# Performance work log

Hardware: AMD Instinct MI355X
Metric: run time of the kernel (lower is better)

Reference implementation:

```python
import jax, jax.numpy as jnp
import numpy as np

PENETRATION_W = 10.0
STABILITY_W = 1.0
ENERGY_W = 0.1
MIN_DIST = 0.05

B, T, N, D = 16, 100, 128, 3

def setup_inputs() -> dict:
    key = jax.random.key(0)
    k1, k2, k3 = jax.random.split(key, 3)
    trajectories = jax.random.normal(k1, (B, T, N, D), dtype=jnp.float32)
    velocities = jax.random.normal(k2, (B, T, N, D), dtype=jnp.float32)
    forces = jax.random.normal(k3, (B, T, N, D), dtype=jnp.float32)
    return {"trajectories": trajectories, "velocities": velocities, "forces": forces}

def _penetration_loss(trajectories):
    b, t, n, _ = trajectories.shape
    pos = trajectories[..., :3]                                   # [B,T,N,3]
    diff = pos[:, :, :, None, :] - pos[:, :, None, :, :]          # [B,T,N,N,3]
    d2 = jnp.sum(diff * diff, axis=-1)                            # [B,T,N,N]
    mask = jnp.triu(jnp.ones((n, n), dtype=bool), k=1)            # strictly i<j
    # avoid sqrt(0) on diagonal for safe gradients; masked out below
    dist = jnp.sqrt(jnp.where(mask, d2, 1.0))
    pen = jax.nn.relu(MIN_DIST - dist) * mask                     # [B,T,N,N]
    # original: sum over (t, i<j) of mean over batch
    total = jnp.mean(jnp.sum(pen, axis=(1, 2, 3)))
    return total / (t * n * (n - 1) / 2)

def _stability_loss(velocities):
    return jnp.mean(jnp.linalg.norm(velocities[:, -5:], axis=-1))

def _energy_loss(positions, velocities, forces):
    kinetic_start = 0.5 * jnp.mean(jnp.sum(velocities[:, 0] ** 2, axis=-1))
    kinetic_end = 0.5 * jnp.mean(jnp.sum(velocities[:, -1] ** 2, axis=-1))
    displacements = positions[:, 1:] - positions[:, :-1]
    work = jnp.mean(jnp.sum(forces[:, :-1] * displacements, axis=-1))
    return jnp.abs(kinetic_end - kinetic_start - work)

def reference(trajectories, velocities, forces):
    loss = PENETRATION_W * _penetration_loss(trajectories)
    loss = loss + STABILITY_W * _stability_loss(velocities)
    loss = loss + ENERGY_W * _energy_loss(trajectories, velocities, forces)
    return loss
```

## Files before the change

### kernel.cpp

```cpp
#include <hip/hip_runtime.h>
#include <math.h>

constexpr int B = 16, T = 100, N = 128;
constexpr float MIN_DIST  = 0.05f;
constexpr float MIN_DIST2 = MIN_DIST * MIN_DIST;

constexpr int THREADS      = 256;
constexpr int PEN_BLOCKS   = B * T;
constexpr int MISC_BLOCKS  = 160;
constexpr int TOTAL_BLOCKS = PEN_BLOCKS + MISC_BLOCKS;

constexpr int PER_B = T * N * 3;
constexpr int PER_T = N * 3;

constexpr int WORK_V4_PER_B = (T - 1) * N * 3 / 4;
constexpr int WORK_V4 = B * WORK_V4_PER_B;
constexpr int KE_V4_PER_SLICE = N * 3 / 4;
constexpr int KE_V4  = 2 * B * KE_V4_PER_SLICE;
constexpr int STAB_V = B * 5 * N;
constexpr int MISC_TOTAL = WORK_V4 + STAB_V + KE_V4;

constexpr int WORK_N = B * (T - 1) * N;

constexpr int WORK_OFF = 1600, STAB_OFF = 1760, KE0_OFF = 1920, KE1_OFF = 2080;

__device__ __forceinline__ float wave_sum(float v) {
#pragma unroll
    for (int off = 32; off > 0; off >>= 1) v += __shfl_down(v, off, 64);
    return v;
}

__global__ __launch_bounds__(THREADS) void physics_fused(
    const float* __restrict__ traj, const float* __restrict__ vel,
    const float* __restrict__ frc, float* __restrict__ ws)
{
    __shared__ float4 spos[N];
    __shared__ float  sraw[PER_T];
    __shared__ float  red[4][4];

    const int tid  = threadIdx.x;
    const int bid  = blockIdx.x;
    const int lane = tid & 63;
    const int wv   = tid >> 6;

    if (bid >= MISC_BLOCKS) {
        const int pb = bid - MISC_BLOCKS;
        if (tid < PER_T / 4)
            ((float4*)sraw)[tid] = ((const float4*)traj)[pb * (PER_T / 4) + tid];
        __syncthreads();
        if (tid < N)
            spos[tid] = make_float4(sraw[tid * 3], sraw[tid * 3 + 1], sraw[tid * 3 + 2], 0.f);
        __syncthreads();

        const int i    = tid & (N - 1);
        const int half = tid >> 7;
        const float4 pi = spos[i];
        float s = 0.f;
        const int k0 = 1 + half * 32;
        const int k1 = 32 + half * 31;
#pragma unroll 8
        for (int k = k0; k <= k1; ++k) {
            const int j = (i + k) & (N - 1);
            const float4 pj = spos[j];
            const float dx = pi.x - pj.x, dy = pi.y - pj.y, dz = pi.z - pj.z;
            const float d2 = dx * dx + dy * dy + dz * dz;
            const bool h = d2 < MIN_DIST2;
            if (__builtin_expect(__any(h), 0))
                if (h) s += MIN_DIST - sqrtf(d2);
        }
        if (half) {
            const float4 pj = spos[(i + 64) & (N - 1)];
            const float dx = pi.x - pj.x, dy = pi.y - pj.y, dz = pi.z - pj.z;
            const float d2 = dx * dx + dy * dy + dz * dz;
            const bool h = (d2 < MIN_DIST2) & (i < 64);
            if (__builtin_expect(__any(h), 0))
                if (h) s += MIN_DIST - sqrtf(d2);
        }
        float w = wave_sum(s);
        if (lane == 0) red[0][wv] = w;
        __syncthreads();
        if (tid == 0)
            ws[pb] = red[0][0] + red[0][1] + red[0][2] + red[0][3];
    } else {
        const int mb = bid;
        const float4* t4 = (const float4*)traj;
        const float4* f4 = (const float4*)frc;
        const float4* v4 = (const float4*)vel;
        float sw = 0.f, ss = 0.f, k0 = 0.f, k1 = 0.f;
        const int stride = MISC_BLOCKS * THREADS;
        for (int v = mb * THREADS + tid; v < MISC_TOTAL; v += stride) {
            if (v < WORK_V4) {
                const int b = v / WORK_V4_PER_B;
                const int r = v - b * WORK_V4_PER_B;
                const int base = b * (PER_B / 4) + r;
                const float4 f  = f4[base];
                const float4 t0 = t4[base];
                const float4 t1 = t4[base + PER_T / 4];
                sw += f.x * (t1.x - t0.x) + f.y * (t1.y - t0.y)
                    + f.z * (t1.z - t0.z) + f.w * (t1.w - t0.w);
            } else if (v < WORK_V4 + STAB_V) {
                const int s2 = v - WORK_V4;
                const int b  = s2 / 640;
                const int r  = s2 - b * 640;
                const int e  = b * PER_B + 95 * PER_T + r * 3;
                const float vx = vel[e], vy = vel[e + 1], vz = vel[e + 2];
                ss += sqrtf(vx * vx + vy * vy + vz * vz);
            } else {
                const int s2    = v - WORK_V4 - STAB_V;
                const int which = s2 / 1536;
                const int rr    = s2 - which * 1536;
                const int b     = rr / KE_V4_PER_SLICE;
                const int r     = rr - b * KE_V4_PER_SLICE;
                const float4 q  = v4[b * (PER_B / 4) + which * (99 * PER_T / 4) + r];
                const float k   = q.x * q.x + q.y * q.y + q.z * q.z + q.w * q.w;
                if (which) k1 += k; else k0 += k;
            }
        }
        float vals[4] = {sw, ss, k0, k1};
#pragma unroll
        for (int vv = 0; vv < 4; ++vv) {
            float w = wave_sum(vals[vv]);
            if (lane == 0) red[vv][wv] = w;
        }
        __syncthreads();
        if (tid == 0) {
            ws[WORK_OFF + mb] = red[0][0] + red[0][1] + red[0][2] + red[0][3];
            ws[STAB_OFF + mb] = red[1][0] + red[1][1] + red[1][2] + red[1][3];
            ws[KE0_OFF  + mb] = red[2][0] + red[2][1] + red[2][2] + red[2][3];
            ws[KE1_OFF  + mb] = red[3][0] + red[3][1] + red[3][2] + red[3][3];
        }
    }
}

__global__ __launch_bounds__(256) void physics_finalize(
    const float* __restrict__ ws, float* __restrict__ out)
{
    __shared__ float redP[4], redM[4];
    const int tid = threadIdx.x, lane = tid & 63, wv = tid >> 6;

    float p = 0.f;
    for (int i = tid; i < PEN_BLOCKS; i += 256) p += ws[i];

    const int base = WORK_OFF + 160 * wv;
    float m = ws[base + lane] + ws[base + 64 + lane]
            + (lane < 32 ? ws[base + 128 + lane] : 0.f);

    p = wave_sum(p);
    m = wave_sum(m);
    if (lane == 0) { redP[wv] = p; redM[wv] = m; }
    __syncthreads();

    if (tid == 0) {
        const float pen = redP[0] + redP[1] + redP[2] + redP[3];
        const float wk = redM[0], st = redM[1], k0 = redM[2], k1 = redM[3];
        const float pen_loss  = pen / (float)((long long)B * T * (N * (N - 1) / 2));
        const float stab_loss = st / (float)STAB_V;
        const float ke_s = 0.5f * k0 / (float)(B * N);
        const float ke_e = 0.5f * k1 / (float)(B * N);
        const float work = wk / (float)WORK_N;
        out[0] = 10.0f * pen_loss + stab_loss + 0.1f * fabsf(ke_e - ke_s - work);
    }
}

extern "C" void kernel_launch(void* const* d_in, const int* in_sizes, int n_in,
                              void* d_out, int out_size, void* d_ws, size_t ws_size,
                              hipStream_t stream) {
    const float* traj = (const float*)d_in[0];
    const float* vel  = (const float*)d_in[1];
    const float* frc  = (const float*)d_in[2];
    float* out = (float*)d_out;
    float* ws  = (float*)d_ws;

    physics_fused<<<TOTAL_BLOCKS, THREADS, 0, stream>>>(traj, vel, frc, ws);
    physics_finalize<<<1, 256, 0, stream>>>(ws, out);
}
```

Baseline: 68.36 us.

## Merge penetration and misc work per block; use cooperative grid sync for finalize

Restructures the grid to 800 uniform blocks, each handling two time-slices of pairwise penetration plus one element of the work/stability/kinetic reductions. Global loads for the misc terms are issued before the pair loop so their latency overlaps with compute. The separate finalize kernel is replaced by a cooperative launch with a grid-wide sync and a single-block final reduction, with a two-kernel fallback if the cooperative launch fails. This removes one kernel launch and the load imbalance between block types, but adds grid-sync cost and relies on all 800 blocks being co-resident.

```diff
diff --git a/kernel.cpp b/kernel.cpp
--- a/kernel.cpp
+++ b/kernel.cpp
@@ -1,14 +1,15 @@
 #include <hip/hip_runtime.h>
+#include <hip/hip_cooperative_groups.h>
 #include <math.h>
+
+namespace cg = cooperative_groups;
 
 constexpr int B = 16, T = 100, N = 128;
 constexpr float MIN_DIST  = 0.05f;
 constexpr float MIN_DIST2 = MIN_DIST * MIN_DIST;
 
-constexpr int THREADS      = 256;
-constexpr int PEN_BLOCKS   = B * T;
-constexpr int MISC_BLOCKS  = 160;
-constexpr int TOTAL_BLOCKS = PEN_BLOCKS + MISC_BLOCKS;
+constexpr int THREADS = 256;
+constexpr int G       = 800;
 
 constexpr int PER_B = T * N * 3;
 constexpr int PER_T = N * 3;
@@ -22,141 +23,181 @@
 
 constexpr int WORK_N = B * (T - 1) * N;
 
-constexpr int WORK_OFF = 1600, STAB_OFF = 1760, KE0_OFF = 1920, KE1_OFF = 2080;
-
 __device__ __forceinline__ float wave_sum(float v) {
 #pragma unroll
     for (int off = 32; off > 0; off >>= 1) v += __shfl_down(v, off, 64);
     return v;
 }
 
-__global__ __launch_bounds__(THREADS) void physics_fused(
+template <bool COOP>
+__global__ __launch_bounds__(THREADS, 4) void physics_one(
     const float* __restrict__ traj, const float* __restrict__ vel,
-    const float* __restrict__ frc, float* __restrict__ ws)
+    const float* __restrict__ frc, float* __restrict__ ws,
+    float* __restrict__ out)
 {
-    __shared__ float4 spos[N];
-    __shared__ float  sraw[PER_T];
-    __shared__ float  red[4][4];
+    __shared__ float  sraw[2 * PER_T];
+    __shared__ float4 spos[2][N];
+    __shared__ float  red[5][4];
 
     const int tid  = threadIdx.x;
     const int bid  = blockIdx.x;
     const int lane = tid & 63;
     const int wv   = tid >> 6;
 
-    if (bid >= MISC_BLOCKS) {
-        const int pb = bid - MISC_BLOCKS;
-        if (tid < PER_T / 4)
-            ((float4*)sraw)[tid] = ((const float4*)traj)[pb * (PER_T / 4) + tid];
-        __syncthreads();
-        if (tid < N)
-            spos[tid] = make_float4(sraw[tid * 3], sraw[tid * 3 + 1], sraw[tid * 3 + 2], 0.f);
-        __syncthreads();
-
-        const int i    = tid & (N - 1);
-        const int half = tid >> 7;
-        const float4 pi = spos[i];
-        float s = 0.f;
-        const int k0 = 1 + half * 32;
-        const int k1 = 32 + half * 31;
+    if (tid < 192) {
+        const int s  = tid >= 96;
+        const int r  = tid - s * 96;
+        const int pb = bid + s * G;
+        ((float4*)sraw)[tid] = ((const float4*)traj)[pb * (PER_T / 4) + r];
+    }
+    __syncthreads();
+    {
+        const int s = tid >> 7, p = tid & (N - 1);
+        const float* rb = sraw + s * PER_T;
+        spos[s][p] = make_float4(rb[p * 3], rb[p * 3 + 1], rb[p * 3 + 2], 0.f);
+    }
+    __syncthreads();
+
+    const int v = bid * THREADS + tid;
+    int cat = 3, which = 0;
+    float4 mf, mt0, mt1;
+    float  e0 = 0.f, e1 = 0.f, e2 = 0.f;
+    {
+        const float4* t4 = (const float4*)traj;
+        const float4* f4 = (const float4*)frc;
+        const float4* v4 = (const float4*)vel;
+        if (v < WORK_V4) {
+            cat = 0;
+            const int b = v / WORK_V4_PER_B;
+            const int r = v - b * WORK_V4_PER_B;
+            const int base = b * (PER_B / 4) + r;
+            mf  = f4[base];
+            mt0 = t4[base];
+            mt1 = t4[base + PER_T / 4];
+        } else if (v < WORK_V4 + STAB_V) {
+            cat = 1;
+            const int s2 = v - WORK_V4;
+            const int b  = s2 / 640;
+            const int r  = s2 - b * 640;
+            const int e  = b * PER_B + 95 * PER_T + r * 3;
+            e0 = vel[e]; e1 = vel[e + 1]; e2 = vel[e + 2];
+        } else if (v < MISC_TOTAL) {
+            cat = 2;
+            const int s2 = v - WORK_V4 - STAB_V;
+            which        = s2 / 1536;
+            const int rr = s2 - which * 1536;
+            const int b  = rr / KE_V4_PER_SLICE;
+            const int r  = rr - b * KE_V4_PER_SLICE;
+            mf = v4[b * (PER_B / 4) + which * (99 * PER_T / 4) + r];
+        }
+    }
+
+    const int i    = tid & (N - 1);
+    const int half = tid >> 7;
+    const int k0   = 1 + half * 32;
+    const int k1   = 32 + half * 31;
+    float pen = 0.f;
+#pragma unroll
+    for (int s = 0; s < 2; ++s) {
+        const float4 pi = spos[s][i];
 #pragma unroll 8
         for (int k = k0; k <= k1; ++k) {
             const int j = (i + k) & (N - 1);
-            const float4 pj = spos[j];
+            const float4 pj = spos[s][j];
             const float dx = pi.x - pj.x, dy = pi.y - pj.y, dz = pi.z - pj.z;
             const float d2 = dx * dx + dy * dy + dz * dz;
             const bool h = d2 < MIN_DIST2;
             if (__builtin_expect(__any(h), 0))
-                if (h) s += MIN_DIST - sqrtf(d2);
+                if (h) pen += MIN_DIST - sqrtf(d2);
         }
         if (half) {
-            const float4 pj = spos[(i + 64) & (N - 1)];
+            const float4 pj = spos[s][(i + 64) & (N - 1)];
             const float dx = pi.x - pj.x, dy = pi.y - pj.y, dz = pi.z - pj.z;
             const float d2 = dx * dx + dy * dy + dz * dz;
             const bool h = (d2 < MIN_DIST2) & (i < 64);
             if (__builtin_expect(__any(h), 0))
-                if (h) s += MIN_DIST - sqrtf(d2);
+                if (h) pen += MIN_DIST - sqrtf(d2);
         }
-        float w = wave_sum(s);
-        if (lane == 0) red[0][wv] = w;
-        __syncthreads();
-        if (tid == 0)
-            ws[pb] = red[0][0] + red[0][1] + red[0][2] + red[0][3];
-    } else {
-        const int mb = bid;
-        const float4* t4 = (const float4*)traj;
-        const float4* f4 = (const float4*)frc;
-        const float4* v4 = (const float4*)vel;
-        float sw = 0.f, ss = 0.f, k0 = 0.f, k1 = 0.f;
-        const int stride = MISC_BLOCKS * THREADS;
-        for (int v = mb * THREADS + tid; v < MISC_TOTAL; v += stride) {
-            if (v < WORK_V4) {
-                const int b = v / WORK_V4_PER_B;
-                const int r = v - b * WORK_V4_PER_B;
-                const int base = b * (PER_B / 4) + r;
-                const float4 f  = f4[base];
-                const float4 t0 = t4[base];
-                const float4 t1 = t4[base + PER_T / 4];
-                sw += f.x * (t1.x - t0.x) + f.y * (t1.y - t0.y)
-                    + f.z * (t1.z - t0.z) + f.w * (t1.w - t0.w);
-            } else if (v < WORK_V4 + STAB_V) {
-                const int s2 = v - WORK_V4;
-                const int b  = s2 / 640;
-                const int r  = s2 - b * 640;
-                const int e  = b * PER_B + 95 * PER_T + r * 3;
-                const float vx = vel[e], vy = vel[e + 1], vz = vel[e + 2];
-                ss += sqrtf(vx * vx + vy * vy + vz * vz);
-            } else {
-                const int s2    = v - WORK_V4 - STAB_V;
-                const int which = s2 / 1536;
-                const int rr    = s2 - which * 1536;
-                const int b     = rr / KE_V4_PER_SLICE;
-                const int r     = rr - b * KE_V4_PER_SLICE;
-                const float4 q  = v4[b * (PER_B / 4) + which * (99 * PER_T / 4) + r];
-                const float k   = q.x * q.x + q.y * q.y + q.z * q.z + q.w * q.w;
-                if (which) k1 += k; else k0 += k;
-            }
-        }
-        float vals[4] = {sw, ss, k0, k1};
-#pragma unroll
-        for (int vv = 0; vv < 4; ++vv) {
-            float w = wave_sum(vals[vv]);
-            if (lane == 0) red[vv][wv] = w;
-        }
-        __syncthreads();
-        if (tid == 0) {
-            ws[WORK_OFF + mb] = red[0][0] + red[0][1] + red[0][2] + red[0][3];
-            ws[STAB_OFF + mb] = red[1][0] + red[1][1] + red[1][2] + red[1][3];
-            ws[KE0_OFF  + mb] = red[2][0] + red[2][1] + red[2][2] + red[2][3];
-            ws[KE1_OFF  + mb] = red[3][0] + red[3][1] + red[3][2] + red[3][3];
-        }
-    }
-}
-
-__global__ __launch_bounds__(256) void physics_finalize(
+    }
+
+    float sw = 0.f, ss = 0.f, ka = 0.f, kb = 0.f;
+    if (cat == 0) {
+        sw = mf.x * (mt1.x - mt0.x) + mf.y * (mt1.y - mt0.y)
+           + mf.z * (mt1.z - mt0.z) + mf.w * (mt1.w - mt0.w);
+    } else if (cat == 1) {
+        ss = sqrtf(e0 * e0 + e1 * e1 + e2 * e2);
+    } else if (cat == 2) {
+        const float k = mf.x * mf.x + mf.y * mf.y + mf.z * mf.z + mf.w * mf.w;
+        if (which) kb = k; else ka = k;
+    }
+
+    float vals[5] = {pen, sw, ss, ka, kb};
+#pragma unroll
+    for (int q = 0; q < 5; ++q) {
+        const float w = wave_sum(vals[q]);
+        if (lane == 0) red[q][wv] = w;
+    }
+    __syncthreads();
+    if (tid < 5)
+        ws[tid * G + bid] = red[tid][0] + red[tid][1] + red[tid][2] + red[tid][3];
+
+    if constexpr (!COOP) return;
+
+    cg::this_grid().sync();
+    if (bid != 0) return;
+
+    float acc[5] = {0.f, 0.f, 0.f, 0.f, 0.f};
+    for (int idx = tid; idx < G; idx += THREADS) {
+#pragma unroll
+        for (int q = 0; q < 5; ++q) acc[q] += ws[q * G + idx];
+    }
+#pragma unroll
+    for (int q = 0; q < 5; ++q) {
+        const float w = wave_sum(acc[q]);
+        if (lane == 0) red[q][wv] = w;
+    }
+    __syncthreads();
+    if (tid == 0) {
+        const float pen_t = red[0][0] + red[0][1] + red[0][2] + red[0][3];
+        const float wk    = red[1][0] + red[1][1] + red[1][2] + red[1][3];
+        const float st    = red[2][0] + red[2][1] + red[2][2] + red[2][3];
+        const float k0s   = red[3][0] + red[3][1] + red[3][2] + red[3][3];
+        const float k1s   = red[4][0] + red[4][1] + red[4][2] + red[4][3];
+        const float pen_loss  = pen_t / (float)((long long)B * T * (N * (N - 1) / 2));
+        const float stab_loss = st / (float)STAB_V;
+        const float ke_s = 0.5f * k0s / (float)(B * N);
+        const float ke_e = 0.5f * k1s / (float)(B * N);
+        const float work = wk / (float)WORK_N;
+        out[0] = 10.0f * pen_loss + stab_loss + 0.1f * fabsf(ke_e - ke_s - work);
+    }
+}
+
+__global__ __launch_bounds__(THREADS) void physics_fin(
     const float* __restrict__ ws, float* __restrict__ out)
 {
-    __shared__ float redP[4], redM[4];
+    __shared__ float red[5][4];
     const int tid = threadIdx.x, lane = tid & 63, wv = tid >> 6;
-
-    float p = 0.f;
-    for (int i = tid; i < PEN_BLOCKS; i += 256) p += ws[i];
-
-    const int base = WORK_OFF + 160 * wv;
-    float m = ws[base + lane] + ws[base + 64 + lane]
-            + (lane < 32 ? ws[base + 128 + lane] : 0.f);
-
-    p = wave_sum(p);
-    m = wave_sum(m);
-    if (lane == 0) { redP[wv] = p; redM[wv] = m; }
-    __syncthreads();
-
+    float acc[5] = {0.f, 0.f, 0.f, 0.f, 0.f};
+    for (int idx = tid; idx < G; idx += THREADS) {
+#pragma unroll
+        for (int q = 0; q < 5; ++q) acc[q] += ws[q * G + idx];
+    }
+#pragma unroll
+    for (int q = 0; q < 5; ++q) {
+        const float w = wave_sum(acc[q]);
+        if (lane == 0) red[q][wv] = w;
+    }
+    __syncthreads();
     if (tid == 0) {
-        const float pen = redP[0] + redP[1] + redP[2] + redP[3];
-        const float wk = redM[0], st = redM[1], k0 = redM[2], k1 = redM[3];
-        const float pen_loss  = pen / (float)((long long)B * T * (N * (N - 1) / 2));
+        const float pen_t = red[0][0] + red[0][1] + red[0][2] + red[0][3];
+        const float wk    = red[1][0] + red[1][1] + red[1][2] + red[1][3];
+        const float st    = red[2][0] + red[2][1] + red[2][2] + red[2][3];
+        const float k0s   = red[3][0] + red[3][1] + red[3][2] + red[3][3];
+        const float k1s   = red[4][0] + red[4][1] + red[4][2] + red[4][3];
+        const float pen_loss  = pen_t / (float)((long long)B * T * (N * (N - 1) / 2));
         const float stab_loss = st / (float)STAB_V;
-        const float ke_s = 0.5f * k0 / (float)(B * N);
-        const float ke_e = 0.5f * k1 / (float)(B * N);
+        const float ke_s = 0.5f * k0s / (float)(B * N);
+        const float ke_e = 0.5f * k1s / (float)(B * N);
         const float work = wk / (float)WORK_N;
         out[0] = 10.0f * pen_loss + stab_loss + 0.1f * fabsf(ke_e - ke_s - work);
     }
@@ -171,6 +212,11 @@
     float* out = (float*)d_out;
     float* ws  = (float*)d_ws;
 
-    physics_fused<<<TOTAL_BLOCKS, THREADS, 0, stream>>>(traj, vel, frc, ws);
-    physics_finalize<<<1, 256, 0, stream>>>(ws, out);
-}
+    void* args[] = {(void*)&traj, (void*)&vel, (void*)&frc, (void*)&ws, (void*)&out};
+    const hipError_t err = hipLaunchCooperativeKernel(
+        (const void*)physics_one<true>, dim3(G), dim3(THREADS), args, 0, stream);
+    if (err != hipSuccess) {
+        physics_one<false><<<G, THREADS, 0, stream>>>(traj, vel, frc, ws, out);
+        physics_fin<<<1, THREADS, 0, stream>>>(ws, out);
+    }
+}
```

New measurement: 126.3 us. 84.7% more time.
